# Kernel optimization log

Measured on AMD Instinct MI355X. Metric: run time of the kernel, lower is better.

## Reference

```python
import jax, jax.numpy as jnp
import numpy as np

N_NODES = 100000
N_EDGES = 1600000
IN_CH = 64 * 2  # 128


def setup_inputs() -> dict:
    key = jax.random.key(0)
    ks = jax.random.split(key, 10)
    x = jax.random.normal(ks[0], (N_NODES, IN_CH), dtype=jnp.float32)
    edge_index = jax.random.randint(ks[1], (2, N_EDGES), 0, N_NODES, dtype=jnp.int64)
    # PyTorch Linear default init scale ~ 1/sqrt(fan_in); plain normals are fine for a numeric reference
    W1 = jax.random.normal(ks[2], (IN_CH, 64), dtype=jnp.float32) / np.sqrt(IN_CH)
    b1 = jax.random.normal(ks[3], (64,), dtype=jnp.float32) * 0.01
    W2 = jax.random.normal(ks[4], (64, 64), dtype=jnp.float32) / np.sqrt(64)
    b2 = jax.random.normal(ks[5], (64,), dtype=jnp.float32) * 0.01
    W3 = jax.random.normal(ks[6], (64, 16), dtype=jnp.float32) / np.sqrt(64)
    b3 = jax.random.normal(ks[7], (16,), dtype=jnp.float32) * 0.01
    W4 = jax.random.normal(ks[8], (16, 1), dtype=jnp.float32) / np.sqrt(16)
    b4 = jax.random.normal(ks[9], (1,), dtype=jnp.float32) * 0.01
    return {"x": x, "edge_index": edge_index, "W1": W1, "b1": b1, "W2": W2, "b2": b2,
            "W3": W3, "b3": b3, "W4": W4, "b4": b4}


def _gin_agg(h, src, dst, n):
    # GINConv (eps=0, add aggregation): x_i + sum_{j->i} x_j
    return h + jax.ops.segment_sum(h[src], dst, num_segments=n)


def reference(x, edge_index, W1, b1, W2, b2, W3, b3, W4, b4):
    src, dst = edge_index[0], edge_index[1]
    n = x.shape[0]
    h = jax.nn.relu(_gin_agg(x, src, dst, n) @ W1 + b1)   # conv1 + relu -> [N, 64]
    h = jax.nn.relu(_gin_agg(h, src, dst, n) @ W2 + b2)   # conv2 + relu -> [N, 64]
    h = jax.nn.relu(h @ W3 + b3)                          # lin1 + relu  -> [N, 16]
    return h @ W4 + b4                                    # lin2         -> [N, 1]
```

## Files before the change

kernel.cpp:

```cpp
#include <hip/hip_runtime.h>
#include <hip/hip_fp16.h>

#define N_NODES 100000
#define N_EDGES 1600000
#define NBUCK 196
#define BUCAP 10240
#define P1_EDGES 8192
#define NP1 196
#define CURPAD 32

__global__ __launch_bounds__(256) void k_zero_cur(int* __restrict__ cursor) {
    if (threadIdx.x < NBUCK) cursor[threadIdx.x * CURPAD] = 0;
}

__global__ __launch_bounds__(1024) void k_p1(const int* __restrict__ ei,
                                             int* __restrict__ cursor,
                                             int* __restrict__ bArr) {
    __shared__ int hist[NBUCK];
    const int tid = threadIdx.x;
    if (tid < NBUCK) hist[tid] = 0;

    const int eb = blockIdx.x * P1_EDGES;
    int d[8], s[8];
    #pragma unroll
    for (int j = 0; j < 2; ++j) {
        const int e = eb + j * 4096 + tid * 4;
        if (e < N_EDGES) {
            int4 dd = *(const int4*)&ei[N_EDGES + e];
            int4 ss = *(const int4*)&ei[e];
            d[j*4+0] = dd.x; d[j*4+1] = dd.y; d[j*4+2] = dd.z; d[j*4+3] = dd.w;
            s[j*4+0] = ss.x; s[j*4+1] = ss.y; s[j*4+2] = ss.z; s[j*4+3] = ss.w;
        } else {
            d[j*4+0] = -1; d[j*4+1] = -1; d[j*4+2] = -1; d[j*4+3] = -1;
            s[j*4+0] = 0;  s[j*4+1] = 0;  s[j*4+2] = 0;  s[j*4+3] = 0;
        }
    }
    __syncthreads();
    #pragma unroll
    for (int j = 0; j < 8; ++j)
        if (d[j] >= 0) atomicAdd(&hist[d[j] >> 9], 1);
    __syncthreads();
    if (tid < NBUCK) {
        int c = hist[tid];
        int base = atomicAdd(&cursor[tid * CURPAD], c);
        hist[tid] = base;
    }
    __syncthreads();
    #pragma unroll
    for (int j = 0; j < 8; ++j)
        if (d[j] >= 0) {
            int bk  = d[j] >> 9;
            int pos = atomicAdd(&hist[bk], 1);
            if (pos < BUCAP)
                bArr[bk * BUCAP + pos] = ((d[j] & 511) << 17) | s[j];
        }
}

__global__ __launch_bounds__(1024) void k_p2(const int* __restrict__ bArr,
                                             const int* __restrict__ cursor,
                                             int* __restrict__ srcS,
                                             int* __restrict__ off) {
    __shared__ int hist[512];
    __shared__ int wtot[8];
    __shared__ int curL[NBUCK];
    __shared__ int ordered[BUCAP];
    const int tid = threadIdx.x;
    const int b   = blockIdx.x;
    if (tid < 512)   hist[tid] = 0;
    if (tid < NBUCK) curL[tid] = cursor[tid * CURPAD];
    __syncthreads();

    int n = curL[b]; if (n > BUCAP) n = BUCAP;
    int gBase = 0;
    for (int j = 0; j < NBUCK; ++j) gBase += (j < b) ? curL[j] : 0;

    int pk[10];
    #pragma unroll
    for (int j = 0; j < 10; ++j) {
        int i = tid + j * 1024;
        pk[j] = (i < n) ? bArr[b * BUCAP + i] : -1;
    }
    #pragma unroll
    for (int j = 0; j < 10; ++j)
        if (pk[j] >= 0) atomicAdd(&hist[pk[j] >> 17], 1);
    __syncthreads();

    int v = 0, incl = 0;
    if (tid < 512) {
        v = hist[tid]; incl = v;
        #pragma unroll
        for (int dd = 1; dd < 64; dd <<= 1) {
            int t = __shfl_up(incl, dd, 64);
            if ((tid & 63) >= dd) incl += t;
        }
        if ((tid & 63) == 63) wtot[tid >> 6] = incl;
    }
    __syncthreads();
    if (tid < 512) {
        int add = 0;
        #pragma unroll
        for (int w = 0; w < 8; ++w) add += (w < (tid >> 6)) ? wtot[w] : 0;
        int ex = add + incl - v;
        hist[tid] = ex;
        int node = b * 512 + tid;
        if (node < N_NODES) off[node] = gBase + ex;
    }
    if (b == NBUCK - 1 && tid == 0) off[N_NODES] = N_EDGES;
    __syncthreads();

    #pragma unroll
    for (int j = 0; j < 10; ++j)
        if (pk[j] >= 0) {
            int dl  = pk[j] >> 17;
            int pos = atomicAdd(&hist[dl], 1);
            ordered[pos] = pk[j] & 0x1FFFF;
        }
    __syncthreads();
    for (int i = tid; i < n; i += 1024) srcS[gBase + i] = ordered[i];
}

__device__ __forceinline__ float2 gather_core(const int* __restrict__ off,
                                              const int* __restrict__ srcS,
                                              const __half* __restrict__ y16,
                                              int node, int lane) {
    const int hf   = lane >> 5;
    const int ln32 = lane & 31;
    const int beg = off[node];
    const int end = off[node + 1];

    float2 acc = {0.f, 0.f};
    if (hf == 0) {
        __half2 hv = *(const __half2*)&y16[((size_t)node << 6) + (ln32 << 1)];
        float2 f = __half22float2(hv);
        acc.x = f.x; acc.y = f.y;
    }

    int i = beg;
    while (i < end) {
        const int rem  = end - i;
        const int take = rem < 64 ? rem : 64;
        int idx = i + lane;
        if (idx > end - 1) idx = end - 1;
        const int sv = srcS[idx];
        int j = 0;
        for (; j + 16 <= take; j += 16) {
            const int s0 = __shfl(sv, j + 0  + hf), s1 = __shfl(sv, j + 2  + hf);
            const int s2 = __shfl(sv, j + 4  + hf), s3 = __shfl(sv, j + 6  + hf);
            const int s4 = __shfl(sv, j + 8  + hf), s5 = __shfl(sv, j + 10 + hf);
            const int s6 = __shfl(sv, j + 12 + hf), s7 = __shfl(sv, j + 14 + hf);
            const __half2 h0 = *(const __half2*)&y16[((size_t)s0 << 6) + (ln32 << 1)];
            const __half2 h1 = *(const __half2*)&y16[((size_t)s1 << 6) + (ln32 << 1)];
            const __half2 h2 = *(const __half2*)&y16[((size_t)s2 << 6) + (ln32 << 1)];
            const __half2 h3 = *(const __half2*)&y16[((size_t)s3 << 6) + (ln32 << 1)];
            const __half2 h4 = *(const __half2*)&y16[((size_t)s4 << 6) + (ln32 << 1)];
            const __half2 h5 = *(const __half2*)&y16[((size_t)s5 << 6) + (ln32 << 1)];
            const __half2 h6 = *(const __half2*)&y16[((size_t)s6 << 6) + (ln32 << 1)];
            const __half2 h7 = *(const __half2*)&y16[((size_t)s7 << 6) + (ln32 << 1)];
            float2 f0 = __half22float2(h0), f1 = __half22float2(h1);
            float2 f2 = __half22float2(h2), f3 = __half22float2(h3);
            float2 f4 = __half22float2(h4), f5 = __half22float2(h5);
            float2 f6 = __half22float2(h6), f7 = __half22float2(h7);
            acc.x += ((f0.x + f1.x) + (f2.x + f3.x)) + ((f4.x + f5.x) + (f6.x + f7.x));
            acc.y += ((f0.y + f1.y) + (f2.y + f3.y)) + ((f4.y + f5.y) + (f6.y + f7.y));
        }
        for (; j + 2 <= take; j += 2) {
            const int s = __shfl(sv, j + hf);
            const __half2 hv = *(const __half2*)&y16[((size_t)s << 6) + (ln32 << 1)];
            float2 f = __half22float2(hv);
            acc.x += f.x; acc.y += f.y;
        }
        if (j < take) {
            const int s = __shfl(sv, j);
            if (hf == 0) {
                const __half2 hv = *(const __half2*)&y16[((size_t)s << 6) + (ln32 << 1)];
                float2 f = __half22float2(hv);
                acc.x += f.x; acc.y += f.y;
            }
        }
        i += take;
    }
    return acc;
}

__global__ __launch_bounds__(256) void k_gather_h1(const int* __restrict__ off,
                                                   const int* __restrict__ srcS,
                                                   const __half* __restrict__ y16,
                                                   const float* __restrict__ b1,
                                                   __half* __restrict__ h16) {
    const int node = blockIdx.x * 4 + (threadIdx.x >> 6);
    if (node >= N_NODES) return;
    const int lane = threadIdx.x & 63;
    const int hf = lane >> 5, ln32 = lane & 31;
    float2 bb = {0.f, 0.f};
    if (hf == 0) bb = *(const float2*)&b1[ln32 * 2];

    float2 acc = gather_core(off, srcS, y16, node, lane);
    acc.x += __shfl_xor(acc.x, 32, 64);
    acc.y += __shfl_xor(acc.y, 32, 64);
    if (hf == 0) {
        float hx = fmaxf(acc.x + bb.x, 0.f);
        float hy = fmaxf(acc.y + bb.y, 0.f);
        *(__half2*)&h16[((size_t)node << 6) + (ln32 << 1)] = __floats2half2_rn(hx, hy);
    }
}

__global__ __launch_bounds__(256) void k_gather_tail(const int* __restrict__ off,
                                                     const int* __restrict__ srcS,
                                                     const __half* __restrict__ y16,
                                                     const float* __restrict__ b2,
                                                     const float* __restrict__ W3,
                                                     const float* __restrict__ b3,
                                                     const float* __restrict__ W4,
                                                     const float* __restrict__ b4,
                                                     float* __restrict__ out) {
    __shared__ float sh2[4][64];
    const int wv   = threadIdx.x >> 6;
    const int node = blockIdx.x * 4 + wv;
    if (node >= N_NODES) return;
    const int lane = threadIdx.x & 63;
    const int hf = lane >> 5, ln32 = lane & 31;

    const int jj = lane & 15, pp = lane >> 4;
    float w3r[16];
    #pragma unroll
    for (int k = 0; k < 16; ++k) w3r[k] = W3[(pp * 16 + k) * 16 + jj];
    const float b3j = b3[jj], w4j = W4[jj], b4v = b4[0];
    float2 bb = {0.f, 0.f};
    if (hf == 0) bb = *(const float2*)&b2[ln32 * 2];

    float2 acc = gather_core(off, srcS, y16, node, lane);
    acc.x += __shfl_xor(acc.x, 32, 64);
    acc.y += __shfl_xor(acc.y, 32, 64);
    if (hf == 0) {
        float hx = fmaxf(acc.x + bb.x, 0.f);
        float hy = fmaxf(acc.y + bb.y, 0.f);
        *(float2*)&sh2[wv][ln32 * 2] = make_float2(hx, hy);
    }
    const float4 hA = *(const float4*)&sh2[wv][pp * 16 + 0];
    const float4 hB = *(const float4*)&sh2[wv][pp * 16 + 4];
    const float4 hC = *(const float4*)&sh2[wv][pp * 16 + 8];
    const float4 hD = *(const float4*)&sh2[wv][pp * 16 + 12];
    float part = hA.x * w3r[0]  + hA.y * w3r[1]  + hA.z * w3r[2]  + hA.w * w3r[3]
               + hB.x * w3r[4]  + hB.y * w3r[5]  + hB.z * w3r[6]  + hB.w * w3r[7]
               + hC.x * w3r[8]  + hC.y * w3r[9]  + hC.z * w3r[10] + hC.w * w3r[11]
               + hD.x * w3r[12] + hD.y * w3r[13] + hD.z * w3r[14] + hD.w * w3r[15];
    part += __shfl_xor(part, 16, 64);
    part += __shfl_xor(part, 32, 64);
    float o = fmaxf(part + b3j, 0.f) * w4j;
    o += __shfl_xor(o, 1, 64);
    o += __shfl_xor(o, 2, 64);
    o += __shfl_xor(o, 4, 64);
    o += __shfl_xor(o, 8, 64);
    if (lane == 0) out[node] = o + b4v;
}

#define FMA16()                                                       \
    do {                                                              \
        acc0.x += a.x * w.x; acc0.y += a.x * w.y;                     \
        acc0.z += a.x * w.z; acc0.w += a.x * w.w;                     \
        acc1.x += a.y * w.x; acc1.y += a.y * w.y;                     \
        acc1.z += a.y * w.z; acc1.w += a.y * w.w;                     \
        acc2.x += a.z * w.x; acc2.y += a.z * w.y;                     \
        acc2.z += a.z * w.z; acc2.w += a.z * w.w;                     \
        acc3.x += a.w * w.x; acc3.y += a.w * w.y;                     \
        acc3.z += a.w * w.z; acc3.w += a.w * w.w;                     \
    } while (0)

__device__ __forceinline__ void store_h4(__half* p, float4 a) {
    union { __half2 h[2]; uint2 u; } P;
    P.h[0] = __floats2half2_rn(a.x, a.y);
    P.h[1] = __floats2half2_rn(a.z, a.w);
    *(uint2*)p = P.u;
}

__global__ __launch_bounds__(256) void k_mm1(const float* __restrict__ x,
                                             const float* __restrict__ W1,
                                             __half* __restrict__ y16) {
    __shared__ float sW[128 * 64];
    __shared__ float sxT[128 * 68];
    const int tid  = threadIdx.x;
    const int row0 = blockIdx.x * 64;
    #pragma unroll
    for (int i = tid * 4; i < 128 * 64; i += 1024)
        *(float4*)&sW[i] = *(const float4*)&W1[i];
    #pragma unroll 8
    for (int i = tid; i < 64 * 128; i += 256) {
        int m = i >> 7, k = i & 127;
        int r = row0 + m; if (r >= N_NODES) r = N_NODES - 1;
        sxT[k * 68 + m] = x[(size_t)r * 128 + k];
    }
    __syncthreads();
    const int tx = tid & 15;
    const int ty = tid >> 4;
    float4 acc0 = {0.f,0.f,0.f,0.f}, acc1 = {0.f,0.f,0.f,0.f};
    float4 acc2 = {0.f,0.f,0.f,0.f}, acc3 = {0.f,0.f,0.f,0.f};
    #pragma unroll 4
    for (int k = 0; k < 128; ++k) {
        float4 a = *(const float4*)&sxT[k * 68 + ty * 4];
        float4 w = *(const float4*)&sW[k * 64 + tx * 4];
        FMA16();
    }
    const int rb = row0 + ty * 4;
    if (rb + 0 < N_NODES) store_h4(&y16[(size_t)(rb + 0) * 64 + tx * 4], acc0);
    if (rb + 1 < N_NODES) store_h4(&y16[(size_t)(rb + 1) * 64 + tx * 4], acc1);
    if (rb + 2 < N_NODES) store_h4(&y16[(size_t)(rb + 2) * 64 + tx * 4], acc2);
    if (rb + 3 < N_NODES) store_h4(&y16[(size_t)(rb + 3) * 64 + tx * 4], acc3);
}

__global__ __launch_bounds__(256) void k_mm2(const __half* __restrict__ h16,
                                             const float* __restrict__ W2,
                                             __half* __restrict__ y16) {
    __shared__ float sW[64 * 64];
    __shared__ float shT[64 * 68];
    const int tid  = threadIdx.x;
    const int row0 = blockIdx.x * 64;
    #pragma unroll
    for (int i = tid * 4; i < 64 * 64; i += 1024)
        *(float4*)&sW[i] = *(const float4*)&W2[i];
    #pragma unroll
    for (int i = tid * 2; i < 64 * 64; i += 512) {
        int m = i >> 6, k = i & 63;
        int r = row0 + m; if (r >= N_NODES) r = N_NODES - 1;
        __half2 hv = *(const __half2*)&h16[(size_t)r * 64 + k];
        float2 f = __half22float2(hv);
        shT[k * 68 + m]       = f.x;
        shT[(k + 1) * 68 + m] = f.y;
    }
    __syncthreads();
    const int tx = tid & 15;
    const int ty = tid >> 4;
    float4 acc0 = {0.f,0.f,0.f,0.f}, acc1 = {0.f,0.f,0.f,0.f};
    float4 acc2 = {0.f,0.f,0.f,0.f}, acc3 = {0.f,0.f,0.f,0.f};
    #pragma unroll 4
    for (int k = 0; k < 64; ++k) {
        float4 a = *(const float4*)&shT[k * 68 + ty * 4];
        float4 w = *(const float4*)&sW[k * 64 + tx * 4];
        FMA16();
    }
    const int rb = row0 + ty * 4;
    if (rb + 0 < N_NODES) store_h4(&y16[(size_t)(rb + 0) * 64 + tx * 4], acc0);
    if (rb + 1 < N_NODES) store_h4(&y16[(size_t)(rb + 1) * 64 + tx * 4], acc1);
    if (rb + 2 < N_NODES) store_h4(&y16[(size_t)(rb + 2) * 64 + tx * 4], acc2);
    if (rb + 3 < N_NODES) store_h4(&y16[(size_t)(rb + 3) * 64 + tx * 4], acc3);
}

extern "C" void kernel_launch(void* const* d_in, const int* in_sizes, int n_in,
                              void* d_out, int out_size, void* d_ws, size_t ws_size,
                              hipStream_t stream) {
    const float* x  = (const float*)d_in[0];
    const int*   ei = (const int*)d_in[1];
    const float* W1 = (const float*)d_in[2];
    const float* b1 = (const float*)d_in[3];
    const float* W2 = (const float*)d_in[4];
    const float* b2 = (const float*)d_in[5];
    const float* W3 = (const float*)d_in[6];
    const float* b3 = (const float*)d_in[7];
    const float* W4 = (const float*)d_in[8];
    const float* b4 = (const float*)d_in[9];
    float* out = (float*)d_out;

    __half* h16    = (__half*)d_ws;
    __half* y16    = h16 + (size_t)N_NODES * 64;
    int*    off    = (int*)(y16 + (size_t)N_NODES * 64);
    int*    srcS   = off + N_NODES + 4;
    int*    cursor = srcS + N_EDGES;
    int*    bArr   = (int*)d_ws;

    const int mmBlocks  = (N_NODES + 63) / 64;
    const int aggBlocks = (N_NODES + 3) / 4;

    k_zero_cur<<<1, 256, 0, stream>>>(cursor);
    k_p1<<<NP1, 1024, 0, stream>>>(ei, cursor, bArr);
    k_p2<<<NBUCK, 1024, 0, stream>>>(bArr, cursor, srcS, off);

    k_mm1<<<mmBlocks, 256, 0, stream>>>(x, W1, y16);
    k_gather_h1<<<aggBlocks, 256, 0, stream>>>(off, srcS, y16, b1, h16);
    k_mm2<<<mmBlocks, 256, 0, stream>>>(h16, W2, y16);
    k_gather_tail<<<aggBlocks, 256, 0, stream>>>(off, srcS, y16, b2, W3, b3, W4, b4, out);
}
```

Measured before the change: 284.2 us.

## Gather neighbor rows with 16-byte loads across 8 edges per wavefront

The neighbor gather is restructured so each 8-lane group loads a full 128-byte fp16 row segment with uint4 (16B) loads. That puts 8 edges in flight per wavefront instruction instead of 2 edges using 4-byte loads. Partial sums are combined with an xor-shuffle tree across groups. The tail MLP is reworked to use the resulting 8-feature-per-lane layout directly, dropping the shared-memory staging. This trades more shuffle reductions and more accumulator registers for fewer, wider memory instructions in the bandwidth- and latency-bound gather.

Measured after the change: 328.5 us. +15.6%, slower.

```diff
diff --git a/kernel.cpp b/kernel.cpp
--- a/kernel.cpp
+++ b/kernel.cpp
@@ -119,21 +119,31 @@
     for (int i = tid; i < n; i += 1024) srcS[gBase + i] = ordered[i];
 }
 
-__device__ __forceinline__ float2 gather_core(const int* __restrict__ off,
-                                              const int* __restrict__ srcS,
-                                              const __half* __restrict__ y16,
-                                              int node, int lane) {
-    const int hf   = lane >> 5;
-    const int ln32 = lane & 31;
+union UH { unsigned u; __half2 h; };
+struct Acc8 { float2 a0, a1, a2, a3; };
+
+__device__ __forceinline__ void add8(Acc8& A, uint4 q) {
+    UH u0, u1, u2, u3;
+    u0.u = q.x; u1.u = q.y; u2.u = q.z; u3.u = q.w;
+    float2 f0 = __half22float2(u0.h), f1 = __half22float2(u1.h);
+    float2 f2 = __half22float2(u2.h), f3 = __half22float2(u3.h);
+    A.a0.x += f0.x; A.a0.y += f0.y; A.a1.x += f1.x; A.a1.y += f1.y;
+    A.a2.x += f2.x; A.a2.y += f2.y; A.a3.x += f3.x; A.a3.y += f3.y;
+}
+
+__device__ __forceinline__ Acc8 gather_core8(const int* __restrict__ off,
+                                             const int* __restrict__ srcS,
+                                             const __half* __restrict__ y16,
+                                             int node, int lane) {
+    const int g   = lane >> 3;
+    const int s8  = lane & 7;
+    const int bo  = s8 << 3;
     const int beg = off[node];
     const int end = off[node + 1];
 
-    float2 acc = {0.f, 0.f};
-    if (hf == 0) {
-        __half2 hv = *(const __half2*)&y16[((size_t)node << 6) + (ln32 << 1)];
-        float2 f = __half22float2(hv);
-        acc.x = f.x; acc.y = f.y;
-    }
+    Acc8 A = {{0.f,0.f},{0.f,0.f},{0.f,0.f},{0.f,0.f}};
+    if (g == 0)
+        add8(A, *(const uint4*)&y16[((size_t)node << 6) + bo]);
 
     int i = beg;
     while (i < end) {
@@ -143,43 +153,42 @@
         if (idx > end - 1) idx = end - 1;
         const int sv = srcS[idx];
         int j = 0;
+        for (; j + 32 <= take; j += 32) {
+            const int e0 = __shfl(sv, j + g);
+            const int e1 = __shfl(sv, j + 8 + g);
+            const int e2 = __shfl(sv, j + 16 + g);
+            const int e3 = __shfl(sv, j + 24 + g);
+            const uint4 q0 = *(const uint4*)&y16[((size_t)e0 << 6) + bo];
+            const uint4 q1 = *(const uint4*)&y16[((size_t)e1 << 6) + bo];
+            const uint4 q2 = *(const uint4*)&y16[((size_t)e2 << 6) + bo];
+            const uint4 q3 = *(const uint4*)&y16[((size_t)e3 << 6) + bo];
+            add8(A, q0); add8(A, q1); add8(A, q2); add8(A, q3);
+        }
         for (; j + 16 <= take; j += 16) {
-            const int s0 = __shfl(sv, j + 0  + hf), s1 = __shfl(sv, j + 2  + hf);
-            const int s2 = __shfl(sv, j + 4  + hf), s3 = __shfl(sv, j + 6  + hf);
-            const int s4 = __shfl(sv, j + 8  + hf), s5 = __shfl(sv, j + 10 + hf);
-            const int s6 = __shfl(sv, j + 12 + hf), s7 = __shfl(sv, j + 14 + hf);
-            const __half2 h0 = *(const __half2*)&y16[((size_t)s0 << 6) + (ln32 << 1)];
-            const __half2 h1 = *(const __half2*)&y16[((size_t)s1 << 6) + (ln32 << 1)];
-            const __half2 h2 = *(const __half2*)&y16[((size_t)s2 << 6) + (ln32 << 1)];
-            const __half2 h3 = *(const __half2*)&y16[((size_t)s3 << 6) + (ln32 << 1)];
-            const __half2 h4 = *(const __half2*)&y16[((size_t)s4 << 6) + (ln32 << 1)];
-            const __half2 h5 = *(const __half2*)&y16[((size_t)s5 << 6) + (ln32 << 1)];
-            const __half2 h6 = *(const __half2*)&y16[((size_t)s6 << 6) + (ln32 << 1)];
-            const __half2 h7 = *(const __half2*)&y16[((size_t)s7 << 6) + (ln32 << 1)];
-            float2 f0 = __half22float2(h0), f1 = __half22float2(h1);
-            float2 f2 = __half22float2(h2), f3 = __half22float2(h3);
-            float2 f4 = __half22float2(h4), f5 = __half22float2(h5);
-            float2 f6 = __half22float2(h6), f7 = __half22float2(h7);
-            acc.x += ((f0.x + f1.x) + (f2.x + f3.x)) + ((f4.x + f5.x) + (f6.x + f7.x));
-            acc.y += ((f0.y + f1.y) + (f2.y + f3.y)) + ((f4.y + f5.y) + (f6.y + f7.y));
-        }
-        for (; j + 2 <= take; j += 2) {
-            const int s = __shfl(sv, j + hf);
-            const __half2 hv = *(const __half2*)&y16[((size_t)s << 6) + (ln32 << 1)];
-            float2 f = __half22float2(hv);
-            acc.x += f.x; acc.y += f.y;
-        }
-        if (j < take) {
-            const int s = __shfl(sv, j);
-            if (hf == 0) {
-                const __half2 hv = *(const __half2*)&y16[((size_t)s << 6) + (ln32 << 1)];
-                float2 f = __half22float2(hv);
-                acc.x += f.x; acc.y += f.y;
-            }
+            const int e0 = __shfl(sv, j + g);
+            const int e1 = __shfl(sv, j + 8 + g);
+            const uint4 q0 = *(const uint4*)&y16[((size_t)e0 << 6) + bo];
+            const uint4 q1 = *(const uint4*)&y16[((size_t)e1 << 6) + bo];
+            add8(A, q0); add8(A, q1);
+        }
+        for (; j < take; j += 8) {
+            int jj = j + g;
+            const bool vld = (jj < take);
+            if (jj > take - 1) jj = take - 1;
+            const int e = __shfl(sv, jj);
+            const uint4 q = *(const uint4*)&y16[((size_t)e << 6) + bo];
+            if (vld) add8(A, q);
         }
         i += take;
     }
-    return acc;
+    #pragma unroll
+    for (int d = 8; d < 64; d <<= 1) {
+        A.a0.x += __shfl_xor(A.a0.x, d, 64); A.a0.y += __shfl_xor(A.a0.y, d, 64);
+        A.a1.x += __shfl_xor(A.a1.x, d, 64); A.a1.y += __shfl_xor(A.a1.y, d, 64);
+        A.a2.x += __shfl_xor(A.a2.x, d, 64); A.a2.y += __shfl_xor(A.a2.y, d, 64);
+        A.a3.x += __shfl_xor(A.a3.x, d, 64); A.a3.y += __shfl_xor(A.a3.y, d, 64);
+    }
+    return A;
 }
 
 __global__ __launch_bounds__(256) void k_gather_h1(const int* __restrict__ off,
@@ -190,17 +199,20 @@
     const int node = blockIdx.x * 4 + (threadIdx.x >> 6);
     if (node >= N_NODES) return;
     const int lane = threadIdx.x & 63;
-    const int hf = lane >> 5, ln32 = lane & 31;
-    float2 bb = {0.f, 0.f};
-    if (hf == 0) bb = *(const float2*)&b1[ln32 * 2];
-
-    float2 acc = gather_core(off, srcS, y16, node, lane);
-    acc.x += __shfl_xor(acc.x, 32, 64);
-    acc.y += __shfl_xor(acc.y, 32, 64);
-    if (hf == 0) {
-        float hx = fmaxf(acc.x + bb.x, 0.f);
-        float hy = fmaxf(acc.y + bb.y, 0.f);
-        *(__half2*)&h16[((size_t)node << 6) + (ln32 << 1)] = __floats2half2_rn(hx, hy);
+    const int g = lane >> 3, s8 = lane & 7;
+
+    Acc8 A = gather_core8(off, srcS, y16, node, lane);
+
+    if (g == 0) {
+        const float4 bA = *(const float4*)&b1[s8 * 8];
+        const float4 bB = *(const float4*)&b1[s8 * 8 + 4];
+        UH o0, o1, o2, o3;
+        o0.h = __floats2half2_rn(fmaxf(A.a0.x + bA.x, 0.f), fmaxf(A.a0.y + bA.y, 0.f));
+        o1.h = __floats2half2_rn(fmaxf(A.a1.x + bA.z, 0.f), fmaxf(A.a1.y + bA.w, 0.f));
+        o2.h = __floats2half2_rn(fmaxf(A.a2.x + bB.x, 0.f), fmaxf(A.a2.y + bB.y, 0.f));
+        o3.h = __floats2half2_rn(fmaxf(A.a3.x + bB.z, 0.f), fmaxf(A.a3.y + bB.w, 0.f));
+        uint4 q = {o0.u, o1.u, o2.u, o3.u};
+        *(uint4*)&h16[((size_t)node << 6) + (s8 << 3)] = q;
     }
 }
 
@@ -213,45 +225,41 @@
                                                      const float* __restrict__ W4,
                                                      const float* __restrict__ b4,
                                                      float* __restrict__ out) {
-    __shared__ float sh2[4][64];
-    const int wv   = threadIdx.x >> 6;
-    const int node = blockIdx.x * 4 + wv;
+    const int node = blockIdx.x * 4 + (threadIdx.x >> 6);
     if (node >= N_NODES) return;
     const int lane = threadIdx.x & 63;
-    const int hf = lane >> 5, ln32 = lane & 31;
-
-    const int jj = lane & 15, pp = lane >> 4;
-    float w3r[16];
-    #pragma unroll
-    for (int k = 0; k < 16; ++k) w3r[k] = W3[(pp * 16 + k) * 16 + jj];
-    const float b3j = b3[jj], w4j = W4[jj], b4v = b4[0];
-    float2 bb = {0.f, 0.f};
-    if (hf == 0) bb = *(const float2*)&b2[ln32 * 2];
-
-    float2 acc = gather_core(off, srcS, y16, node, lane);
-    acc.x += __shfl_xor(acc.x, 32, 64);
-    acc.y += __shfl_xor(acc.y, 32, 64);
-    if (hf == 0) {
-        float hx = fmaxf(acc.x + bb.x, 0.f);
-        float hy = fmaxf(acc.y + bb.y, 0.f);
-        *(float2*)&sh2[wv][ln32 * 2] = make_float2(hx, hy);
-    }
-    const float4 hA = *(const float4*)&sh2[wv][pp * 16 + 0];
-    const float4 hB = *(const float4*)&sh2[wv][pp * 16 + 4];
-    const float4 hC = *(const float4*)&sh2[wv][pp * 16 + 8];
-    const float4 hD = *(const float4*)&sh2[wv][pp * 16 + 12];
-    float part = hA.x * w3r[0]  + hA.y * w3r[1]  + hA.z * w3r[2]  + hA.w * w3r[3]
-               + hB.x * w3r[4]  + hB.y * w3r[5]  + hB.z * w3r[6]  + hB.w * w3r[7]
-               + hC.x * w3r[8]  + hC.y * w3r[9]  + hC.z * w3r[10] + hC.w * w3r[11]
-               + hD.x * w3r[12] + hD.y * w3r[13] + hD.z * w3r[14] + hD.w * w3r[15];
-    part += __shfl_xor(part, 16, 64);
-    part += __shfl_xor(part, 32, 64);
-    float o = fmaxf(part + b3j, 0.f) * w4j;
-    o += __shfl_xor(o, 1, 64);
-    o += __shfl_xor(o, 2, 64);
-    o += __shfl_xor(o, 4, 64);
-    o += __shfl_xor(o, 8, 64);
-    if (lane == 0) out[node] = o + b4v;
+    const int g = lane >> 3, s8 = lane & 7;
+
+    float w3a[8], w3b[8];
+    #pragma unroll
+    for (int k = 0; k < 8; ++k) {
+        w3a[k] = W3[(s8 * 8 + k) * 16 + g * 2];
+        w3b[k] = W3[(s8 * 8 + k) * 16 + g * 2 + 1];
+    }
+
+    Acc8 A = gather_core8(off, srcS, y16, node, lane);
+
+    const float4 bA = *(const float4*)&b2[s8 * 8];
+    const float4 bB = *(const float4*)&b2[s8 * 8 + 4];
+    const float h0 = fmaxf(A.a0.x + bA.x, 0.f), h1 = fmaxf(A.a0.y + bA.y, 0.f);
+    const float h2 = fmaxf(A.a1.x + bA.z, 0.f), h3 = fmaxf(A.a1.y + bA.w, 0.f);
+    const float h4 = fmaxf(A.a2.x + bB.x, 0.f), h5 = fmaxf(A.a2.y + bB.y, 0.f);
+    const float h6 = fmaxf(A.a3.x + bB.z, 0.f), h7 = fmaxf(A.a3.y + bB.w, 0.f);
+
+    float p0 = h0*w3a[0] + h1*w3a[1] + h2*w3a[2] + h3*w3a[3]
+             + h4*w3a[4] + h5*w3a[5] + h6*w3a[6] + h7*w3a[7];
+    float p1 = h0*w3b[0] + h1*w3b[1] + h2*w3b[2] + h3*w3b[3]
+             + h4*w3b[4] + h5*w3b[5] + h6*w3b[6] + h7*w3b[7];
+    #pragma unroll
+    for (int d = 1; d < 8; d <<= 1) {
+        p0 += __shfl_xor(p0, d, 64);
+        p1 += __shfl_xor(p1, d, 64);
+    }
+    float o = fmaxf(p0 + b3[g * 2], 0.f)     * W4[g * 2]
+            + fmaxf(p1 + b3[g * 2 + 1], 0.f) * W4[g * 2 + 1];
+    #pragma unroll
+    for (int d = 8; d < 64; d <<= 1) o += __shfl_xor(o, d, 64);
+    if (lane == 0) out[node] = o + b4[0];
 }
 
 #define FMA16()                                                       \
```

## Use MFMA f16 matrix instructions for the two dense node-feature matmuls

Applied to the files above, without the earlier changes.

Replaces the scalar FP32 register-tiled GEMMs in k_mm1 and k_mm2 with MFMA 16x16x32 f16 instructions. Each wave computes a 16x64 output tile, reading A rows straight from global memory and B from a transposed f16 copy of the weights in LDS. This drops the per-block transposed staging of x through shared memory and the FMA-bound inner loop. The catch is that x and the weights are rounded to fp16 before multiplication, which lowers precision, and the output stores are now 2-byte scattered writes instead of 8-byte vector stores.

Result: faster. 254.9 us (-10.3%).

```diff
diff --git a/kernel.cpp b/kernel.cpp
--- a/kernel.cpp
+++ b/kernel.cpp
@@ -8,6 +8,9 @@
 #define P1_EDGES 8192
 #define NP1 196
 #define CURPAD 32
+
+typedef _Float16 f16x8 __attribute__((ext_vector_type(8)));
+typedef float    f32x4 __attribute__((ext_vector_type(4)));
 
 __global__ __launch_bounds__(256) void k_zero_cur(int* __restrict__ cursor) {
     if (threadIdx.x < NBUCK) cursor[threadIdx.x * CURPAD] = 0;
@@ -254,94 +257,105 @@
     if (lane == 0) out[node] = o + b4v;
 }
 
-#define FMA16()                                                       \
-    do {                                                              \
-        acc0.x += a.x * w.x; acc0.y += a.x * w.y;                     \
-        acc0.z += a.x * w.z; acc0.w += a.x * w.w;                     \
-        acc1.x += a.y * w.x; acc1.y += a.y * w.y;                     \
-        acc1.z += a.y * w.z; acc1.w += a.y * w.w;                     \
-        acc2.x += a.z * w.x; acc2.y += a.z * w.y;                     \
-        acc2.z += a.z * w.z; acc2.w += a.z * w.w;                     \
-        acc3.x += a.w * w.x; acc3.y += a.w * w.y;                     \
-        acc3.z += a.w * w.z; acc3.w += a.w * w.w;                     \
-    } while (0)
-
-__device__ __forceinline__ void store_h4(__half* p, float4 a) {
-    union { __half2 h[2]; uint2 u; } P;
-    P.h[0] = __floats2half2_rn(a.x, a.y);
-    P.h[1] = __floats2half2_rn(a.z, a.w);
-    *(uint2*)p = P.u;
-}
-
 __global__ __launch_bounds__(256) void k_mm1(const float* __restrict__ x,
                                              const float* __restrict__ W1,
                                              __half* __restrict__ y16) {
-    __shared__ float sW[128 * 64];
-    __shared__ float sxT[128 * 68];
-    const int tid  = threadIdx.x;
-    const int row0 = blockIdx.x * 64;
-    #pragma unroll
-    for (int i = tid * 4; i < 128 * 64; i += 1024)
-        *(float4*)&sW[i] = *(const float4*)&W1[i];
-    #pragma unroll 8
-    for (int i = tid; i < 64 * 128; i += 256) {
-        int m = i >> 7, k = i & 127;
-        int r = row0 + m; if (r >= N_NODES) r = N_NODES - 1;
-        sxT[k * 68 + m] = x[(size_t)r * 128 + k];
-    }
-    __syncthreads();
-    const int tx = tid & 15;
-    const int ty = tid >> 4;
-    float4 acc0 = {0.f,0.f,0.f,0.f}, acc1 = {0.f,0.f,0.f,0.f};
-    float4 acc2 = {0.f,0.f,0.f,0.f}, acc3 = {0.f,0.f,0.f,0.f};
-    #pragma unroll 4
-    for (int k = 0; k < 128; ++k) {
-        float4 a = *(const float4*)&sxT[k * 68 + ty * 4];
-        float4 w = *(const float4*)&sW[k * 64 + tx * 4];
-        FMA16();
-    }
-    const int rb = row0 + ty * 4;
-    if (rb + 0 < N_NODES) store_h4(&y16[(size_t)(rb + 0) * 64 + tx * 4], acc0);
-    if (rb + 1 < N_NODES) store_h4(&y16[(size_t)(rb + 1) * 64 + tx * 4], acc1);
-    if (rb + 2 < N_NODES) store_h4(&y16[(size_t)(rb + 2) * 64 + tx * 4], acc2);
-    if (rb + 3 < N_NODES) store_h4(&y16[(size_t)(rb + 3) * 64 + tx * 4], acc3);
+    __shared__ __half sB[64 * 136];
+    const int tid = threadIdx.x;
+    for (int i = tid * 4; i < 128 * 64; i += 1024) {
+        int k = i >> 6, n = i & 63;
+        float4 w = *(const float4*)&W1[i];
+        sB[(n + 0) * 136 + k] = __float2half(w.x);
+        sB[(n + 1) * 136 + k] = __float2half(w.y);
+        sB[(n + 2) * 136 + k] = __float2half(w.z);
+        sB[(n + 3) * 136 + k] = __float2half(w.w);
+    }
+    __syncthreads();
+    const int wv = tid >> 6, l = tid & 63;
+    const int row0 = blockIdx.x * 64 + wv * 16;
+    int arow = row0 + (l & 15);
+    if (arow >= N_NODES) arow = N_NODES - 1;
+    const int kgrp = (l >> 4) * 8;
+
+    f32x4 acc0 = {0,0,0,0}, acc1 = {0,0,0,0}, acc2 = {0,0,0,0}, acc3 = {0,0,0,0};
+    #pragma unroll
+    for (int ks = 0; ks < 4; ++ks) {
+        const float4 a0 = *(const float4*)&x[(size_t)arow * 128 + ks * 32 + kgrp];
+        const float4 a1 = *(const float4*)&x[(size_t)arow * 128 + ks * 32 + kgrp + 4];
+        f16x8 af;
+        af[0] = (_Float16)a0.x; af[1] = (_Float16)a0.y;
+        af[2] = (_Float16)a0.z; af[3] = (_Float16)a0.w;
+        af[4] = (_Float16)a1.x; af[5] = (_Float16)a1.y;
+        af[6] = (_Float16)a1.z; af[7] = (_Float16)a1.w;
+        union { uint4 u; f16x8 h; } B0, B1, B2, B3;
+        B0.u = *(const uint4*)&sB[(0 * 16 + (l & 15)) * 136 + ks * 32 + kgrp];
+        B1.u = *(const uint4*)&sB[(1 * 16 + (l & 15)) * 136 + ks * 32 + kgrp];
+        B2.u = *(const uint4*)&sB[(2 * 16 + (l & 15)) * 136 + ks * 32 + kgrp];
+        B3.u = *(const uint4*)&sB[(3 * 16 + (l & 15)) * 136 + ks * 32 + kgrp];
+        acc0 = __builtin_amdgcn_mfma_f32_16x16x32_f16(af, B0.h, acc0, 0, 0, 0);
+        acc1 = __builtin_amdgcn_mfma_f32_16x16x32_f16(af, B1.h, acc1, 0, 0, 0);
+        acc2 = __builtin_amdgcn_mfma_f32_16x16x32_f16(af, B2.h, acc2, 0, 0, 0);
+        acc3 = __builtin_amdgcn_mfma_f32_16x16x32_f16(af, B3.h, acc3, 0, 0, 0);
+    }
+    #pragma unroll
+    for (int rr = 0; rr < 4; ++rr) {
+        const int orow = row0 + (l >> 4) * 4 + rr;
+        if (orow < N_NODES) {
+            __half* yp = &y16[(size_t)orow * 64 + (l & 15)];
+            yp[0]  = __float2half(acc0[rr]);
+            yp[16] = __float2half(acc1[rr]);
+            yp[32] = __float2half(acc2[rr]);
+            yp[48] = __float2half(acc3[rr]);
+        }
+    }
 }
 
 __global__ __launch_bounds__(256) void k_mm2(const __half* __restrict__ h16,
                                              const float* __restrict__ W2,
                                              __half* __restrict__ y16) {
-    __shared__ float sW[64 * 64];
-    __shared__ float shT[64 * 68];
-    const int tid  = threadIdx.x;
-    const int row0 = blockIdx.x * 64;
-    #pragma unroll
-    for (int i = tid * 4; i < 64 * 64; i += 1024)
-        *(float4*)&sW[i] = *(const float4*)&W2[i];
-    #pragma unroll
-    for (int i = tid * 2; i < 64 * 64; i += 512) {
-        int m = i >> 6, k = i & 63;
-        int r = row0 + m; if (r >= N_NODES) r = N_NODES - 1;
-        __half2 hv = *(const __half2*)&h16[(size_t)r * 64 + k];
-        float2 f = __half22float2(hv);
-        shT[k * 68 + m]       = f.x;
-        shT[(k + 1) * 68 + m] = f.y;
-    }
-    __syncthreads();
-    const int tx = tid & 15;
-    const int ty = tid >> 4;
-    float4 acc0 = {0.f,0.f,0.f,0.f}, acc1 = {0.f,0.f,0.f,0.f};
-    float4 acc2 = {0.f,0.f,0.f,0.f}, acc3 = {0.f,0.f,0.f,0.f};
-    #pragma unroll 4
-    for (int k = 0; k < 64; ++k) {
-        float4 a = *(const float4*)&shT[k * 68 + ty * 4];
-        float4 w = *(const float4*)&sW[k * 64 + tx * 4];
-        FMA16();
-    }
-    const int rb = row0 + ty * 4;
-    if (rb + 0 < N_NODES) store_h4(&y16[(size_t)(rb + 0) * 64 + tx * 4], acc0);
-    if (rb + 1 < N_NODES) store_h4(&y16[(size_t)(rb + 1) * 64 + tx * 4], acc1);
-    if (rb + 2 < N_NODES) store_h4(&y16[(size_t)(rb + 2) * 64 + tx * 4], acc2);
-    if (rb + 3 < N_NODES) store_h4(&y16[(size_t)(rb + 3) * 64 + tx * 4], acc3);
+    __shared__ __half sB[64 * 72];
+    const int tid = threadIdx.x;
+    for (int i = tid * 4; i < 64 * 64; i += 1024) {
+        int k = i >> 6, n = i & 63;
+        float4 w = *(const float4*)&W2[i];
+        sB[(n + 0) * 72 + k] = __float2half(w.x);
+        sB[(n + 1) * 72 + k] = __float2half(w.y);
+        sB[(n + 2) * 72 + k] = __float2half(w.z);
+        sB[(n + 3) * 72 + k] = __float2half(w.w);
+    }
+    __syncthreads();
+    const int wv = tid >> 6, l = tid & 63;
+    const int row0 = blockIdx.x * 64 + wv * 16;
+    int arow = row0 + (l & 15);
+    if (arow >= N_NODES) arow = N_NODES - 1;
+    const int kgrp = (l >> 4) * 8;
+
+    f32x4 acc0 = {0,0,0,0}, acc1 = {0,0,0,0}, acc2 = {0,0,0,0}, acc3 = {0,0,0,0};
+    #pragma unroll
+    for (int ks = 0; ks < 2; ++ks) {
+        union { uint4 u; f16x8 h; } A;
+        A.u = *(const uint4*)&h16[(size_t)arow * 64 + ks * 32 + kgrp];
+        union { uint4 u; f16x8 h; } B0, B1, B2, B3;
+        B0.u = *(const uint4*)&sB[(0 * 16 + (l & 15)) * 72 + ks * 32 + kgrp];
+        B1.u = *(const uint4*)&sB[(1 * 16 + (l & 15)) * 72 + ks * 32 + kgrp];
+        B2.u = *(const uint4*)&sB[(2 * 16 + (l & 15)) * 72 + ks * 32 + kgrp];
+        B3.u = *(const uint4*)&sB[(3 * 16 + (l & 15)) * 72 + ks * 32 + kgrp];
+        acc0 = __builtin_amdgcn_mfma_f32_16x16x32_f16(A.h, B0.h, acc0, 0, 0, 0);
+        acc1 = __builtin_amdgcn_mfma_f32_16x16x32_f16(A.h, B1.h, acc1, 0, 0, 0);
+        acc2 = __builtin_amdgcn_mfma_f32_16x16x32_f16(A.h, B2.h, acc2, 0, 0, 0);
+        acc3 = __builtin_amdgcn_mfma_f32_16x16x32_f16(A.h, B3.h, acc3, 0, 0, 0);
+    }
+    #pragma unroll
+    for (int rr = 0; rr < 4; ++rr) {
+        const int orow = row0 + (l >> 4) * 4 + rr;
+        if (orow < N_NODES) {
+            __half* yp = &y16[(size_t)orow * 64 + (l & 15)];
+            yp[0]  = __float2half(acc0[rr]);
+            yp[16] = __float2half(acc1[rr]);
+            yp[32] = __float2half(acc2[rr]);
+            yp[48] = __float2half(acc3[rr]);
+        }
+    }
 }
 
 extern "C" void kernel_launch(void* const* d_in, const int* in_sizes, int n_in,
```
